# Performance work log

Measured on AMD Instinct MI355X. Metric: run time of the kernel, lower is better.

## Reference

```python
import jax, jax.numpy as jnp
import numpy as np

NUM_GRAPHS = 2048  # graph.batch_size
EPS = 1e-6


def setup_inputs() -> dict:
    key = jax.random.key(0)
    k1, k2 = jax.random.split(key)
    N, D = 1000000, 128
    feat = jax.random.normal(k1, (N, D), dtype=jnp.float32)
    segment_ids = jnp.sort(jax.random.randint(k2, (N,), 0, NUM_GRAPHS)).astype(jnp.int64)
    weight = jnp.ones((D,), dtype=jnp.float32)
    bias = jnp.zeros((D,), dtype=jnp.float32)
    mean_scale = jnp.ones((D,), dtype=jnp.float32)
    return {"feat": feat, "segment_ids": segment_ids, "weight": weight,
            "bias": bias, "mean_scale": mean_scale}


def reference(feat, segment_ids, weight, bias, mean_scale):
    # counts per graph ( == graph.batch_num_nodes() ). Clamp to 1 so that
    # empty segments (which never contribute to the output) don't produce NaNs.
    counts = jnp.maximum(
        jax.ops.segment_sum(jnp.ones_like(segment_ids, dtype=feat.dtype),
                            segment_ids, num_segments=NUM_GRAPHS), 1.0)
    inv_counts = (1.0 / counts)[:, None]                      # [B, 1]

    # per-graph mean: scatter_add then divide by segment size
    mean = jax.ops.segment_sum(feat, segment_ids, num_segments=NUM_GRAPHS) * inv_counts  # [B, D]
    sub = feat - mean[segment_ids] * mean_scale               # [N, D]

    # per-graph std of the mean-shifted features
    var = jax.ops.segment_sum(sub * sub, segment_ids, num_segments=NUM_GRAPHS) * inv_counts
    std = jnp.sqrt(var + EPS)                                 # [B, D]

    return weight * sub / std[segment_ids] + bias
```

## Files before the change

### kernel.cpp

```cpp
#include <hip/hip_runtime.h>

#define D 128
#define NSEG 2048
#define EPSV 1e-6f
#define BLOCK 256
#define QCH 8
#define CPRF 32
#define RG (BLOCK/QCH)
#define WAVES (BLOCK/64)
#define MAXK 16

typedef float f32x4 __attribute__((ext_vector_type(4)));

__global__ __launch_bounds__(BLOCK, 4) void graphnorm_fused(
    const float* __restrict__ feat,
    const int* __restrict__ seg,
    const float* __restrict__ weight,
    const float* __restrict__ bias,
    const float* __restrict__ mean_scale,
    float* __restrict__ out,
    int N)
{
    const int bid = blockIdx.x;
    const int s = bid >> 2;
    const int q = bid & 3;
    __shared__ int s_range[2];
    __shared__ f32x4 s_sum[WAVES][QCH];
    __shared__ f32x4 s_sq[WAVES][QCH];
    __shared__ f32x4 s_a[QCH];
    __shared__ f32x4 s_b[QCH];

    const int t = threadIdx.x;

    if (t < 2) {
        int target = s + t;
        int lo = 0, hi = N;
        while (lo < hi) {
            int mid = (lo + hi) >> 1;
            if (seg[mid] < target) lo = mid + 1; else hi = mid;
        }
        s_range[t] = lo;
    }
    __syncthreads();
    const int start = s_range[0];
    const int end   = s_range[1];

    const int c = t & (QCH - 1);
    const int g = t >> 3;
    const int chunk = q * QCH + c;

    const f32x4* feat4 = reinterpret_cast<const f32x4*>(feat);
    f32x4* out4 = reinterpret_cast<f32x4*>(out);

    f32x4 buf[MAXK];
    #pragma unroll
    for (int k = 0; k < MAXK; ++k) {
        const int r = start + g + k * RG;
        if (r < end) buf[k] = feat4[r * CPRF + chunk];
    }

    f32x4 s0 = 0.f, q0 = 0.f;
    #pragma unroll
    for (int k = 0; k < MAXK; ++k) {
        const int r = start + g + k * RG;
        if (r < end) {
            s0 += buf[k];
            q0 += buf[k] * buf[k];
        }
    }

    const int tail_base = start + g + MAXK * RG;
    for (int r = tail_base; r < end; r += RG) {
        f32x4 v = feat4[r * CPRF + chunk];
        s0 += v;
        q0 += v * v;
    }

    #pragma unroll
    for (int i = 0; i < 4; ++i) {
        s0[i] += __shfl_xor(s0[i], 8);
        s0[i] += __shfl_xor(s0[i], 16);
        s0[i] += __shfl_xor(s0[i], 32);
        q0[i] += __shfl_xor(q0[i], 8);
        q0[i] += __shfl_xor(q0[i], 16);
        q0[i] += __shfl_xor(q0[i], 32);
    }

    const int w    = t >> 6;
    const int lane = t & 63;
    if (lane < QCH) {
        s_sum[w][lane] = s0;
        s_sq[w][lane]  = q0;
    }
    __syncthreads();

    if (t < QCH) {
        f32x4 sm = s_sum[0][t];
        f32x4 sg = s_sq[0][t];
        #pragma unroll
        for (int i = 1; i < WAVES; ++i) {
            sm += s_sum[i][t];
            sg += s_sq[i][t];
        }
        const float cnt = (float)max(end - start, 1);
        const float inv = 1.0f / cnt;
        const int wc = q * QCH + t;
        const f32x4 wv  = reinterpret_cast<const f32x4*>(weight)[wc];
        const f32x4 bi  = reinterpret_cast<const f32x4*>(bias)[wc];
        const f32x4 msc = reinterpret_cast<const f32x4*>(mean_scale)[wc];
        f32x4 A, B;
        #pragma unroll
        for (int i = 0; i < 4; ++i) {
            float mean = sm[i] * inv;
            float ms   = mean * msc[i];
            float var  = fmaxf(sg[i] * inv - 2.f * mean * ms + ms * ms, 0.f);
            float istd = rsqrtf(var + EPSV);
            A[i] = wv[i] * istd;
            B[i] = bi[i] - A[i] * ms;
        }
        s_a[t] = A;
        s_b[t] = B;
    }
    __syncthreads();

    const f32x4 A = s_a[c];
    const f32x4 B = s_b[c];

    #pragma unroll
    for (int k = 0; k < MAXK; ++k) {
        const int r = start + g + k * RG;
        if (r < end)
            __builtin_nontemporal_store(A * buf[k] + B, &out4[r * CPRF + chunk]);
    }
    for (int r = tail_base; r < end; r += RG) {
        f32x4 v = feat4[r * CPRF + chunk];
        __builtin_nontemporal_store(A * v + B, &out4[r * CPRF + chunk]);
    }
}

extern "C" void kernel_launch(void* const* d_in, const int* in_sizes, int n_in,
                              void* d_out, int out_size, void* d_ws, size_t ws_size,
                              hipStream_t stream) {
    const float* feat       = (const float*)d_in[0];
    const int*   seg        = (const int*)d_in[1];
    const float* weight     = (const float*)d_in[2];
    const float* bias       = (const float*)d_in[3];
    const float* mean_scale = (const float*)d_in[4];
    float* out = (float*)d_out;

    const int N = in_sizes[0] / D;

    graphnorm_fused<<<NSEG * 4, BLOCK, 0, stream>>>(
        feat, seg, weight, bias, mean_scale, out, N);
}
```

Measured before the change: 200.9 us.

## Precompute segment offsets in separate kernel and split features over eight blocks per segment

Segment boundary binary searches move from every block into a small pre-pass kernel that writes offsets to workspace. The main kernel now launches eight blocks per segment, each covering four float4 chunks, instead of four blocks covering eight. The register buffer is halved and the occupancy hint raised to six blocks. Every thread now computes the scale and shift itself, which removes a shared-memory round trip and a barrier. The cost is a second kernel launch, and segments larger than the smaller buffer fall back to re-reading features from global memory.

```diff
diff --git a/kernel.cpp b/kernel.cpp
--- a/kernel.cpp
+++ b/kernel.cpp
@@ -4,50 +4,49 @@
 #define NSEG 2048
 #define EPSV 1e-6f
 #define BLOCK 256
-#define QCH 8
+#define QCH 4
+#define NQ 8
 #define CPRF 32
 #define RG (BLOCK/QCH)
 #define WAVES (BLOCK/64)
-#define MAXK 16
+#define MAXK 8
 
 typedef float f32x4 __attribute__((ext_vector_type(4)));
 
-__global__ __launch_bounds__(BLOCK, 4) void graphnorm_fused(
+__global__ void seg_bounds(const int* __restrict__ seg, int* __restrict__ offs, int N) {
+    const int i = blockIdx.x * blockDim.x + threadIdx.x;
+    if (i <= NSEG) {
+        int lo = 0, hi = N;
+        while (lo < hi) {
+            int mid = (lo + hi) >> 1;
+            if (seg[mid] < i) lo = mid + 1; else hi = mid;
+        }
+        offs[i] = lo;
+    }
+}
+
+__global__ __launch_bounds__(BLOCK, 6) void graphnorm_fused(
     const float* __restrict__ feat,
-    const int* __restrict__ seg,
+    const int* __restrict__ offs,
     const float* __restrict__ weight,
     const float* __restrict__ bias,
     const float* __restrict__ mean_scale,
-    float* __restrict__ out,
-    int N)
+    float* __restrict__ out)
 {
     const int bid = blockIdx.x;
-    const int s = bid >> 2;
-    const int q = bid & 3;
-    __shared__ int s_range[2];
+    const int s = bid >> 3;
+    const int q = bid & 7;
+
+    const int start = offs[s];
+    const int end   = offs[s + 1];
+
+    const int t = threadIdx.x;
+    const int c = t & (QCH - 1);
+    const int g = t >> 2;
+    const int chunk = q * QCH + c;
+
     __shared__ f32x4 s_sum[WAVES][QCH];
     __shared__ f32x4 s_sq[WAVES][QCH];
-    __shared__ f32x4 s_a[QCH];
-    __shared__ f32x4 s_b[QCH];
-
-    const int t = threadIdx.x;
-
-    if (t < 2) {
-        int target = s + t;
-        int lo = 0, hi = N;
-        while (lo < hi) {
-            int mid = (lo + hi) >> 1;
-            if (seg[mid] < target) lo = mid + 1; else hi = mid;
-        }
-        s_range[t] = lo;
-    }
-    __syncthreads();
-    const int start = s_range[0];
-    const int end   = s_range[1];
-
-    const int c = t & (QCH - 1);
-    const int g = t >> 3;
-    const int chunk = q * QCH + c;
 
     const f32x4* feat4 = reinterpret_cast<const f32x4*>(feat);
     f32x4* out4 = reinterpret_cast<f32x4*>(out);
@@ -78,9 +77,11 @@
 
     #pragma unroll
     for (int i = 0; i < 4; ++i) {
+        s0[i] += __shfl_xor(s0[i], 4);
         s0[i] += __shfl_xor(s0[i], 8);
         s0[i] += __shfl_xor(s0[i], 16);
         s0[i] += __shfl_xor(s0[i], 32);
+        q0[i] += __shfl_xor(q0[i], 4);
         q0[i] += __shfl_xor(q0[i], 8);
         q0[i] += __shfl_xor(q0[i], 16);
         q0[i] += __shfl_xor(q0[i], 32);
@@ -94,37 +95,28 @@
     }
     __syncthreads();
 
-    if (t < QCH) {
-        f32x4 sm = s_sum[0][t];
-        f32x4 sg = s_sq[0][t];
-        #pragma unroll
-        for (int i = 1; i < WAVES; ++i) {
-            sm += s_sum[i][t];
-            sg += s_sq[i][t];
-        }
-        const float cnt = (float)max(end - start, 1);
-        const float inv = 1.0f / cnt;
-        const int wc = q * QCH + t;
-        const f32x4 wv  = reinterpret_cast<const f32x4*>(weight)[wc];
-        const f32x4 bi  = reinterpret_cast<const f32x4*>(bias)[wc];
-        const f32x4 msc = reinterpret_cast<const f32x4*>(mean_scale)[wc];
-        f32x4 A, B;
-        #pragma unroll
-        for (int i = 0; i < 4; ++i) {
-            float mean = sm[i] * inv;
-            float ms   = mean * msc[i];
-            float var  = fmaxf(sg[i] * inv - 2.f * mean * ms + ms * ms, 0.f);
-            float istd = rsqrtf(var + EPSV);
-            A[i] = wv[i] * istd;
-            B[i] = bi[i] - A[i] * ms;
-        }
-        s_a[t] = A;
-        s_b[t] = B;
+    f32x4 sm = s_sum[0][c];
+    f32x4 sg = s_sq[0][c];
+    #pragma unroll
+    for (int i = 1; i < WAVES; ++i) {
+        sm += s_sum[i][c];
+        sg += s_sq[i][c];
     }
-    __syncthreads();
-
-    const f32x4 A = s_a[c];
-    const f32x4 B = s_b[c];
+    const float cnt = (float)max(end - start, 1);
+    const float inv = 1.0f / cnt;
+    const f32x4 wv  = reinterpret_cast<const f32x4*>(weight)[chunk];
+    const f32x4 bi  = reinterpret_cast<const f32x4*>(bias)[chunk];
+    const f32x4 msc = reinterpret_cast<const f32x4*>(mean_scale)[chunk];
+    f32x4 A, B;
+    #pragma unroll
+    for (int i = 0; i < 4; ++i) {
+        float mean = sm[i] * inv;
+        float ms   = mean * msc[i];
+        float var  = fmaxf(sg[i] * inv - 2.f * mean * ms + ms * ms, 0.f);
+        float istd = rsqrtf(var + EPSV);
+        A[i] = wv[i] * istd;
+        B[i] = bi[i] - A[i] * ms;
+    }
 
     #pragma unroll
     for (int k = 0; k < MAXK; ++k) {
@@ -147,9 +139,11 @@
     const float* bias       = (const float*)d_in[3];
     const float* mean_scale = (const float*)d_in[4];
     float* out = (float*)d_out;
+    int* offs  = (int*)d_ws;
 
     const int N = in_sizes[0] / D;
 
-    graphnorm_fused<<<NSEG * 4, BLOCK, 0, stream>>>(
-        feat, seg, weight, bias, mean_scale, out, N);
+    seg_bounds<<<(NSEG + 1 + 255) / 256, 256, 0, stream>>>(seg, offs, N);
+    graphnorm_fused<<<NSEG * NQ, BLOCK, 0, stream>>>(
+        feat, offs, weight, bias, mean_scale, out);
 }
```

Result: slower. 263.7 us (+31.3%).
